# Performance work log

Measured on AMD Instinct MI355X. Metric: run time of the kernel, lower is better.

Reference implementation:

```python
import jax, jax.numpy as jnp
import numpy as np

D_MODEL = 1024
LAYER_IDX = 5
D_FF = 4096
SPARSITY = 0.9
TOKENS = 8192
IN_UP = D_MODEL * (LAYER_IDX + 1)  # 6144


def _sparse_weight(rng, out_f, in_f, sparsity):
    """Row-wise k-sparse weight matrix mimicking SparseLinear's padded-CSR:
    each output row keeps k = round(in_f*(1-sparsity)) live columns,
    values ~ U(-b, b) with b = 1/sqrt(effective_fan_in)."""
    k = max(1, round(in_f * (1.0 - sparsity)))
    bound = 1.0 / np.sqrt(max(1.0, in_f * (1.0 - sparsity)))
    scores = rng.random((out_f, in_f))
    # top-k per row -> boolean mask
    thresh = np.partition(scores, in_f - k, axis=1)[:, in_f - k][:, None]
    mask = scores >= thresh
    W = (rng.uniform(-bound, bound, (out_f, in_f)).astype(np.float32)) * mask
    return jnp.asarray(W), jnp.asarray(mask)


def setup_inputs() -> dict:
    key = jax.random.key(0)
    x = jax.random.normal(key, (TOKENS, IN_UP), dtype=jnp.float32)
    rng = np.random.default_rng(0)
    W_up, mask_up = _sparse_weight(rng, D_FF, IN_UP, SPARSITY)
    W_down, mask_down = _sparse_weight(rng, D_MODEL, D_FF, SPARSITY)
    return {"ffn_input_cat": x, "W_up": W_up, "W_down": W_down,
            "mask_up": mask_up, "mask_down": mask_down}


def reference(ffn_input_cat, W_up, W_down, mask_up, mask_down):
    # fc_down(gelu(fc_up(x))); SparseLinear == masked dense linear, no bias.
    # torch F.gelu default is the exact (erf) gelu.
    h = jax.nn.gelu(ffn_input_cat @ (W_up * mask_up).T, approximate=False)  # [T, d_ff]
    return h @ (W_down * mask_down).T  # [T, d_model]
```

## Files before the change

### kernel.cpp

```cpp
#include <hip/hip_runtime.h>
#include <cstdint>
#include <cstddef>

typedef unsigned short u16;
typedef __attribute__((ext_vector_type(8))) short  bf16x8;
typedef __attribute__((ext_vector_type(4))) float  f32x4;
typedef __attribute__((ext_vector_type(4))) unsigned short u16x4;

__device__ __forceinline__ u16 f2bf(float f) {
    unsigned u = __float_as_uint(f);
    unsigned r = (u + 0x7FFFu + ((u >> 16) & 1u)) >> 16;
    return (u16)r;
}

__device__ __forceinline__ void async_lds16(const u16* g, u16* l) {
    __builtin_amdgcn_global_load_lds(
        (const __attribute__((address_space(1))) unsigned int*)g,
        (__attribute__((address_space(3))) unsigned int*)l,
        16, 0, 0);
}

__global__ __launch_bounds__(256) void cvt3_kernel(const float* __restrict__ s0, u16* __restrict__ d0, int n0,
                                                   const float* __restrict__ s1, u16* __restrict__ d1, int n1,
                                                   const float* __restrict__ s2, u16* __restrict__ d2, int n2) {
    const int total = n0 + n1 + n2;
    for (int i = blockIdx.x * 256 + threadIdx.x; i < total; i += gridDim.x * 256) {
        const float* s; u16* d; int j = i;
        if (j < n0)            { s = s0; d = d0; }
        else if (j < n0 + n1)  { s = s1; d = d1; j -= n0; }
        else                   { s = s2; d = d2; j -= n0 + n1; }
        float4 a = ((const float4*)s)[j];
        u16x4 o;
        o[0] = f2bf(a.x); o[1] = f2bf(a.y); o[2] = f2bf(a.z); o[3] = f2bf(a.w);
        ((u16x4*)d)[j] = o;
    }
}

#define KHSZ (256 * 32)

template<bool GELU, typename OutT>
__global__ __launch_bounds__(512, 2) void gemm256(const u16* __restrict__ A,
                                                  const u16* __restrict__ B,
                                                  OutT* __restrict__ C,
                                                  int K, int lda, int ldb, int ldc) {
    __shared__ __align__(16) u16 sA[2][2][KHSZ];
    __shared__ __align__(16) u16 sB[2][2][KHSZ];

    const int tid  = threadIdx.x;
    const int wave = tid >> 6;
    const int lane = tid & 63;
    const int quad = lane >> 4;
    const int r16  = lane & 15;

    const int nwg = gridDim.x * gridDim.y;
    int lin = blockIdx.y * gridDim.x + blockIdx.x;
    lin = (lin & 7) * (nwg >> 3) + (lin >> 3);
    const int n0 = (lin % gridDim.x) * 256;
    const int m0 = (lin / gridDim.x) * 256;

    const int wm = (wave >> 2) * 128;
    const int wn = (wave & 3) * 64;

    const int srow = tid >> 2;
    const int scol = ((tid & 3) ^ ((srow >> 1) & 3)) * 8;
    const int ld0  = (wave * 16) * 32;
    const int ld1  = (128 + wave * 16) * 32;

    const u16* gA0 = A + (size_t)(m0 + srow) * lda + scol;
    const u16* gA1 = A + (size_t)(m0 + 128 + srow) * lda + scol;
    const u16* gB0 = B + (size_t)(n0 + srow) * ldb + scol;
    const u16* gB1 = B + (size_t)(n0 + 128 + srow) * ldb + scol;

#define STAGE_A(t, kh) { const int ko_ = (t) * 64 + (kh) * 32; u16* d_ = &sA[(t) & 1][kh][0]; \
        async_lds16(gA0 + ko_, d_ + ld0); async_lds16(gA1 + ko_, d_ + ld1); }
#define STAGE_B(t, kh) { const int ko_ = (t) * 64 + (kh) * 32; u16* d_ = &sB[(t) & 1][kh][0]; \
        async_lds16(gB0 + ko_, d_ + ld0); async_lds16(gB1 + ko_, d_ + ld1); }

    int oA[8], oB[4];
#pragma unroll
    for (int i = 0; i < 8; i++) {
        int ra = wm + i * 16 + r16;
        oA[i] = ra * 32 + ((quad ^ ((ra >> 1) & 3)) << 3);
    }
#pragma unroll
    for (int i = 0; i < 4; i++) {
        int rb = wn + i * 16 + r16;
        oB[i] = rb * 32 + ((quad ^ ((rb >> 1) & 3)) << 3);
    }

    f32x4 acc[8][4] = {};
    const int NT = K / 64;

#define LGKM0 asm volatile("s_waitcnt lgkmcnt(0)" ::: "memory"); __builtin_amdgcn_sched_barrier(0)
#define SBAR  __builtin_amdgcn_sched_barrier(0)
#define MFMA_Q(mbase, AF, BF) \
    __builtin_amdgcn_s_setprio(1); \
    _Pragma("unroll") \
    for (int mi_ = 0; mi_ < 4; mi_++) \
        _Pragma("unroll") \
        for (int ni_ = 0; ni_ < 4; ni_++) \
            acc[(mbase) + mi_][ni_] = __builtin_amdgcn_mfma_f32_16x16x32_bf16( \
                AF[mi_], BF[ni_], acc[(mbase) + mi_][ni_], 0, 0, 0); \
    __builtin_amdgcn_s_setprio(0); \
    __builtin_amdgcn_sched_barrier(0)

    bf16x8 afA[4], afB[4], bfA[4], bfB[4];

    STAGE_A(0, 0); STAGE_B(0, 0);
    STAGE_A(0, 1); STAGE_B(0, 1);
    STAGE_A(1, 0); STAGE_B(1, 0);
    asm volatile("s_waitcnt vmcnt(4)" ::: "memory");
    __builtin_amdgcn_s_barrier();
    SBAR;
    {
        const u16* Ak0 = &sA[0][0][0];
        const u16* Bk0 = &sB[0][0][0];
#pragma unroll
        for (int i = 0; i < 4; i++) {
            afA[i] = *(const bf16x8*)&Ak0[oA[i]];
            bfA[i] = *(const bf16x8*)&Bk0[oB[i]];
        }
    }

    for (int t = 0; t < NT; ++t) {
        const u16* Ak0 = &sA[t & 1][0][0];
        const u16* Ak1 = &sA[t & 1][1][0];
        const u16* Bk1 = &sB[t & 1][1][0];
        const u16* nAk0 = &sA[(t + 1) & 1][0][0];
        const u16* nBk0 = &sB[(t + 1) & 1][0][0];
        const int tn  = (t + 1 < NT) ? t + 1 : t + 1 - NT;
        const int tn2 = (t + 2 < NT) ? t + 2 : t + 2 - NT;

        LGKM0;
        STAGE_A(tn, 1); STAGE_B(tn, 1);
#pragma unroll
        for (int i = 0; i < 4; i++) afB[i] = *(const bf16x8*)&Ak0[oA[4 + i]];
        SBAR;
        MFMA_Q(0, afA, bfA);

        LGKM0;
#pragma unroll
        for (int i = 0; i < 4; i++) {
            afA[i] = *(const bf16x8*)&Ak1[oA[i]];
            bfB[i] = *(const bf16x8*)&Bk1[oB[i]];
        }
        SBAR;
        MFMA_Q(4, afB, bfA);

        __builtin_amdgcn_s_barrier();
        LGKM0;
        STAGE_A(tn2, 0); STAGE_B(tn2, 0);
#pragma unroll
        for (int i = 0; i < 4; i++) afB[i] = *(const bf16x8*)&Ak1[oA[4 + i]];
        SBAR;
        MFMA_Q(0, afA, bfB);

        LGKM0;
        asm volatile("s_waitcnt vmcnt(4)" ::: "memory");
        __builtin_amdgcn_s_barrier();
        SBAR;
#pragma unroll
        for (int i = 0; i < 4; i++) {
            afA[i] = *(const bf16x8*)&nAk0[oA[i]];
            bfA[i] = *(const bf16x8*)&nBk0[oB[i]];
        }
        SBAR;
        MFMA_Q(4, afB, bfB);
    }

#pragma unroll
    for (int mi = 0; mi < 8; mi++) {
#pragma unroll
        for (int r = 0; r < 4; r++) {
            size_t rowoff = (size_t)(m0 + wm + mi * 16 + quad * 4 + r) * ldc;
#pragma unroll
            for (int ni = 0; ni < 4; ni++) {
                int col = n0 + wn + ni * 16 + r16;
                float v = acc[mi][ni][r];
                if constexpr (GELU)
                    v = 0.5f * v * (1.0f + erff(v * 0.70710678118654752f));
                if constexpr (sizeof(OutT) == 2)
                    ((u16*)C)[rowoff + col] = f2bf(v);
                else
                    ((float*)C)[rowoff + col] = v;
            }
        }
    }
}

extern "C" void kernel_launch(void* const* d_in, const int* in_sizes, int n_in,
                              void* d_out, int out_size, void* d_ws, size_t ws_size,
                              hipStream_t stream) {
    const int T   = 8192;
    const int DIN = 6144;
    const int DFF = 4096;
    const int DM  = 1024;

    const float* x  = (const float*)d_in[0];
    const float* wu = (const float*)d_in[1];
    const float* wd = (const float*)d_in[2];

    u16* xb  = (u16*)d_ws;
    u16* wub = xb  + (size_t)T * DIN;
    u16* wdb = wub + (size_t)DFF * DIN;
    u16* hb  = wdb + (size_t)DM * DFF;

    const int n4x  = T * DIN / 4;
    const int n4wu = DFF * DIN / 4;
    const int n4wd = DM * DFF / 4;
    cvt3_kernel<<<8192, 256, 0, stream>>>(x, xb, n4x, wu, wub, n4wu, wd, wdb, n4wd);

    dim3 g1(DFF / 256, T / 256);
    gemm256<true, u16><<<g1, 512, 0, stream>>>(xb, wub, hb, DIN, DIN, DIN, DFF);

    dim3 g2(DM / 256, T / 256);
    gemm256<false, float><<<g2, 512, 0, stream>>>(hb, wdb, (float*)d_out,
                                                  DFF, DFF, DFF, DM);
}
```

Baseline: 955.1 us.

## Use 4-stage K=32 LDS pipeline and 256x128 tiles for down GEMM

Restructures the GEMM main loop from double-buffered K=64 halves into a 4-buffer ring of K=32 slices, with loads issued three steps ahead. Each step now has one barrier, and the loop is unrolled by four so buffer indices are fixed at compile time. The down-projection GEMM switches to 256x128 tiles, doubling its workgroup count from 128 to 256 so more CUs are busy. The costs are a smaller per-barrier compute chunk, more barriers per unit of K, and a templated B-tile size.

```diff
diff --git a/kernel.cpp b/kernel.cpp
--- a/kernel.cpp
+++ b/kernel.cpp
@@ -36,15 +36,18 @@
     }
 }
 
-#define KHSZ (256 * 32)
-
-template<bool GELU, typename OutT>
-__global__ __launch_bounds__(512, 2) void gemm256(const u16* __restrict__ A,
-                                                  const u16* __restrict__ B,
-                                                  OutT* __restrict__ C,
-                                                  int K, int lda, int ldb, int ldc) {
-    __shared__ __align__(16) u16 sA[2][2][KHSZ];
-    __shared__ __align__(16) u16 sB[2][2][KHSZ];
+#define KSTEP 32
+#define ASZ (256 * KSTEP)
+
+template<bool GELU, typename OutT, int BN>
+__global__ __launch_bounds__(512, 2) void gemm_ffn(const u16* __restrict__ A,
+                                                   const u16* __restrict__ B,
+                                                   OutT* __restrict__ C,
+                                                   int K, int lda, int ldb, int ldc) {
+    constexpr int NI = BN / 64;
+    constexpr int SL = (BN == 256) ? 4 : 3;
+    __shared__ __align__(16) u16 sA[4][ASZ];
+    __shared__ __align__(16) u16 sB[4][BN * KSTEP];
 
     const int tid  = threadIdx.x;
     const int wave = tid >> 6;
@@ -55,118 +58,96 @@
     const int nwg = gridDim.x * gridDim.y;
     int lin = blockIdx.y * gridDim.x + blockIdx.x;
     lin = (lin & 7) * (nwg >> 3) + (lin >> 3);
-    const int n0 = (lin % gridDim.x) * 256;
+    const int n0 = (lin % gridDim.x) * BN;
     const int m0 = (lin / gridDim.x) * 256;
 
     const int wm = (wave >> 2) * 128;
-    const int wn = (wave & 3) * 64;
-
-    const int srow = tid >> 2;
-    const int scol = ((tid & 3) ^ ((srow >> 1) & 3)) * 8;
-    const int ld0  = (wave * 16) * 32;
-    const int ld1  = (128 + wave * 16) * 32;
-
-    const u16* gA0 = A + (size_t)(m0 + srow) * lda + scol;
-    const u16* gA1 = A + (size_t)(m0 + 128 + srow) * lda + scol;
-    const u16* gB0 = B + (size_t)(n0 + srow) * ldb + scol;
-    const u16* gB1 = B + (size_t)(n0 + 128 + srow) * ldb + scol;
-
-#define STAGE_A(t, kh) { const int ko_ = (t) * 64 + (kh) * 32; u16* d_ = &sA[(t) & 1][kh][0]; \
-        async_lds16(gA0 + ko_, d_ + ld0); async_lds16(gA1 + ko_, d_ + ld1); }
-#define STAGE_B(t, kh) { const int ko_ = (t) * 64 + (kh) * 32; u16* d_ = &sB[(t) & 1][kh][0]; \
-        async_lds16(gB0 + ko_, d_ + ld0); async_lds16(gB1 + ko_, d_ + ld1); }
-
-    int oA[8], oB[4];
+    const int wn = (wave & 3) * (BN / 4);
+
+    const int sr0 = wave * 16 + (lane >> 2);
+    const int gc0 = (((lane & 3) ^ ((sr0 >> 1) & 3))) * 8;
+    const int ldsw = wave * 512;
+
+    const u16* gA0 = A + (size_t)(m0 + sr0) * lda + gc0;
+    const u16* gA1 = gA0 + (size_t)128 * lda;
+    const u16* gB0 = B + (size_t)(n0 + sr0) * ldb + gc0;
+    const u16* gB1 = gB0 + (size_t)128 * ldb;
+
+#define STAGE(kt, tb) { const int ko_ = (kt) * KSTEP; \
+        async_lds16(gA0 + ko_, &sA[tb][ldsw]); \
+        async_lds16(gA1 + ko_, &sA[tb][4096 + ldsw]); \
+        async_lds16(gB0 + ko_, &sB[tb][ldsw]); \
+        if constexpr (BN == 256) async_lds16(gB1 + ko_, &sB[tb][4096 + ldsw]); }
+
+    int oA[8], oB[NI];
 #pragma unroll
     for (int i = 0; i < 8; i++) {
         int ra = wm + i * 16 + r16;
         oA[i] = ra * 32 + ((quad ^ ((ra >> 1) & 3)) << 3);
     }
 #pragma unroll
-    for (int i = 0; i < 4; i++) {
+    for (int i = 0; i < NI; i++) {
         int rb = wn + i * 16 + r16;
         oB[i] = rb * 32 + ((quad ^ ((rb >> 1) & 3)) << 3);
     }
 
-    f32x4 acc[8][4] = {};
-    const int NT = K / 64;
+    f32x4 acc[8][NI] = {};
+    const int NT = K / KSTEP;
 
 #define LGKM0 asm volatile("s_waitcnt lgkmcnt(0)" ::: "memory"); __builtin_amdgcn_sched_barrier(0)
 #define SBAR  __builtin_amdgcn_sched_barrier(0)
-#define MFMA_Q(mbase, AF, BF) \
+#define VMCNT_STEADY if constexpr (BN == 256) { asm volatile("s_waitcnt vmcnt(8)" ::: "memory"); } \
+                     else { asm volatile("s_waitcnt vmcnt(6)" ::: "memory"); }
+#define MFMA_Q(mb, AF, BF) \
     __builtin_amdgcn_s_setprio(1); \
     _Pragma("unroll") \
     for (int mi_ = 0; mi_ < 4; mi_++) \
         _Pragma("unroll") \
-        for (int ni_ = 0; ni_ < 4; ni_++) \
-            acc[(mbase) + mi_][ni_] = __builtin_amdgcn_mfma_f32_16x16x32_bf16( \
-                AF[mi_], BF[ni_], acc[(mbase) + mi_][ni_], 0, 0, 0); \
+        for (int ni_ = 0; ni_ < NI; ni_++) \
+            acc[(mb) + mi_][ni_] = __builtin_amdgcn_mfma_f32_16x16x32_bf16( \
+                AF[mi_], BF[ni_], acc[(mb) + mi_][ni_], 0, 0, 0); \
     __builtin_amdgcn_s_setprio(0); \
     __builtin_amdgcn_sched_barrier(0)
 
-    bf16x8 afA[4], afB[4], bfA[4], bfB[4];
-
-    STAGE_A(0, 0); STAGE_B(0, 0);
-    STAGE_A(0, 1); STAGE_B(0, 1);
-    STAGE_A(1, 0); STAGE_B(1, 0);
-    asm volatile("s_waitcnt vmcnt(4)" ::: "memory");
+    bf16x8 afA[4], afB[4], bfA[NI], bfB[NI];
+
+    STAGE(0, 0); STAGE(1, 1); STAGE(2, 2);
+    VMCNT_STEADY;
     __builtin_amdgcn_s_barrier();
     SBAR;
-    {
-        const u16* Ak0 = &sA[0][0][0];
-        const u16* Bk0 = &sB[0][0][0];
-#pragma unroll
-        for (int i = 0; i < 4; i++) {
-            afA[i] = *(const bf16x8*)&Ak0[oA[i]];
-            bfA[i] = *(const bf16x8*)&Bk0[oB[i]];
-        }
-    }
-
-    for (int t = 0; t < NT; ++t) {
-        const u16* Ak0 = &sA[t & 1][0][0];
-        const u16* Ak1 = &sA[t & 1][1][0];
-        const u16* Bk1 = &sB[t & 1][1][0];
-        const u16* nAk0 = &sA[(t + 1) & 1][0][0];
-        const u16* nBk0 = &sB[(t + 1) & 1][0][0];
-        const int tn  = (t + 1 < NT) ? t + 1 : t + 1 - NT;
-        const int tn2 = (t + 2 < NT) ? t + 2 : t + 2 - NT;
-
-        LGKM0;
-        STAGE_A(tn, 1); STAGE_B(tn, 1);
-#pragma unroll
-        for (int i = 0; i < 4; i++) afB[i] = *(const bf16x8*)&Ak0[oA[4 + i]];
-        SBAR;
-        MFMA_Q(0, afA, bfA);
-
-        LGKM0;
-#pragma unroll
-        for (int i = 0; i < 4; i++) {
-            afA[i] = *(const bf16x8*)&Ak1[oA[i]];
-            bfB[i] = *(const bf16x8*)&Bk1[oB[i]];
-        }
-        SBAR;
-        MFMA_Q(4, afB, bfA);
-
-        __builtin_amdgcn_s_barrier();
-        LGKM0;
-        STAGE_A(tn2, 0); STAGE_B(tn2, 0);
-#pragma unroll
-        for (int i = 0; i < 4; i++) afB[i] = *(const bf16x8*)&Ak1[oA[4 + i]];
-        SBAR;
-        MFMA_Q(0, afA, bfB);
-
-        LGKM0;
-        asm volatile("s_waitcnt vmcnt(4)" ::: "memory");
-        __builtin_amdgcn_s_barrier();
-        SBAR;
-#pragma unroll
-        for (int i = 0; i < 4; i++) {
-            afA[i] = *(const bf16x8*)&nAk0[oA[i]];
-            bfA[i] = *(const bf16x8*)&nBk0[oB[i]];
-        }
-        SBAR;
-        MFMA_Q(4, afB, bfB);
-    }
+#pragma unroll
+    for (int i = 0; i < 4; i++)  afA[i] = *(const bf16x8*)&sA[0][oA[i]];
+#pragma unroll
+    for (int i = 0; i < NI; i++) bfA[i] = *(const bf16x8*)&sB[0][oB[i]];
+    LGKM0;
+
+#define STEP(T, c, n1, t3, BC, BNx) { \
+        int kt3_ = (T) + 3; if (kt3_ >= NT) kt3_ -= NT; \
+        STAGE(kt3_, t3); \
+        _Pragma("unroll") \
+        for (int i = 0; i < 4; i++) afB[i] = *(const bf16x8*)&sA[c][oA[4 + i]]; \
+        SBAR; \
+        MFMA_Q(0, afA, BC); \
+        LGKM0; \
+        VMCNT_STEADY; \
+        __builtin_amdgcn_s_barrier(); \
+        SBAR; \
+        _Pragma("unroll") \
+        for (int i = 0; i < 4; i++)  afA[i] = *(const bf16x8*)&sA[n1][oA[i]]; \
+        _Pragma("unroll") \
+        for (int i = 0; i < NI; i++) BNx[i] = *(const bf16x8*)&sB[n1][oB[i]]; \
+        SBAR; \
+        MFMA_Q(4, afB, BC); \
+        LGKM0; \
+    }
+
+    for (int t = 0; t < NT; t += 4) {
+        STEP(t + 0, 0, 1, 3, bfA, bfB);
+        STEP(t + 1, 1, 2, 0, bfB, bfA);
+        STEP(t + 2, 2, 3, 1, bfA, bfB);
+        STEP(t + 3, 3, 0, 2, bfB, bfA);
+    }
+    asm volatile("s_waitcnt vmcnt(0)" ::: "memory");
 
 #pragma unroll
     for (int mi = 0; mi < 8; mi++) {
@@ -174,7 +155,7 @@
         for (int r = 0; r < 4; r++) {
             size_t rowoff = (size_t)(m0 + wm + mi * 16 + quad * 4 + r) * ldc;
 #pragma unroll
-            for (int ni = 0; ni < 4; ni++) {
+            for (int ni = 0; ni < NI; ni++) {
                 int col = n0 + wn + ni * 16 + r16;
                 float v = acc[mi][ni][r];
                 if constexpr (GELU)
@@ -211,9 +192,9 @@
     cvt3_kernel<<<8192, 256, 0, stream>>>(x, xb, n4x, wu, wub, n4wu, wd, wdb, n4wd);
 
     dim3 g1(DFF / 256, T / 256);
-    gemm256<true, u16><<<g1, 512, 0, stream>>>(xb, wub, hb, DIN, DIN, DIN, DFF);
-
-    dim3 g2(DM / 256, T / 256);
-    gemm256<false, float><<<g2, 512, 0, stream>>>(hb, wdb, (float*)d_out,
-                                                  DFF, DFF, DFF, DM);
-}
+    gemm_ffn<true, u16, 256><<<g1, 512, 0, stream>>>(xb, wub, hb, DIN, DIN, DIN, DFF);
+
+    dim3 g2(DM / 128, T / 256);
+    gemm_ffn<false, float, 128><<<g2, 512, 0, stream>>>(hb, wdb, (float*)d_out,
+                                                        DFF, DFF, DFF, DM);
+}
```

Result: faster. 888.9 us (-6.9%).
